# Performance work log

Measured on AMD Instinct MI355X. Metric: run time of the kernel, lower is better.

## Reference

```python
import jax, jax.numpy as jnp
import numpy as np
import math

B, S, D = 4, 2048, 1024      # batch, seq, d_model
E, F_EXP = 16, 512           # n_experts_ffn, d_expert_ffn
N_SHARED, K_FFN = 2, 4       # shared experts, routed top-k
N_ROUTED = E - N_SHARED


def setup_inputs() -> dict:
    key = jax.random.key(0)
    k0, k1, k2, k3, k4 = jax.random.split(key, 5)
    token_stream = jax.random.normal(k0, (B, S, D), jnp.float32)
    selection_input = jax.random.normal(k1, (B, S, D), jnp.float32)
    # init per reset_parameters (std_scale = 1.0)
    keys_w = jax.random.normal(k2, (E, D, F_EXP), jnp.float32) / math.sqrt(D)
    values_w = jax.random.normal(k3, (E, F_EXP, D), jnp.float32) / math.sqrt(E * F_EXP)
    expert_sel = jax.random.normal(k4, (E, D), jnp.float32) / math.sqrt(D)
    bias_ffn = jnp.zeros((E,), jnp.float32)  # load-balancing bias buffer
    return {
        "token_stream": token_stream,
        "selection_input": selection_input,
        "keys_w": keys_w,
        "values_w": values_w,
        "expert_sel": expert_sel,
        "bias_ffn": bias_ffn,
    }


def reference(token_stream, selection_input, keys_w, values_w, expert_sel, bias_ffn):
    # ---- routing: sigmoid affinity over all experts ----
    affinity = jax.nn.sigmoid(jnp.einsum("bsd,ed->bse", selection_input, expert_sel))  # [B,S,E]
    # top-k over routed experts (bias only affects ranking, not gathered affinity)
    _, routed_idx = jax.lax.top_k(affinity[..., :N_ROUTED] + bias_ffn[:N_ROUTED], K_FFN)  # [B,S,k]
    shared_idx = jnp.broadcast_to(
        jnp.arange(N_ROUTED, E, dtype=routed_idx.dtype), routed_idx.shape[:-1] + (N_SHARED,)
    )
    sel = jnp.concatenate([routed_idx, shared_idx], axis=-1)  # [B,S,K], K = k + shared
    aff_sel = jnp.take_along_axis(affinity, sel, axis=-1)     # [B,S,K]

    # ---- expert FFN (cvmm = gather / grouped GEMM / weighted scatter) ----
    # dense per-expert key projection, then gather selected experts
    scores_all = jnp.einsum("bsd,edf->bsef", token_stream, keys_w)        # [B,S,E,f]
    scores = jnp.take_along_axis(scores_all, sel[..., None], axis=2)      # [B,S,K,f]
    scores = jax.nn.silu(scores)

    # combine: out = sum_k aff_k * (scores_k @ values[sel_k])
    onehot = jax.nn.one_hot(sel, E, dtype=scores.dtype)                   # [B,S,K,E]
    dispatch = jnp.einsum("bskf,bske->bsef", scores * aff_sel[..., None], onehot)  # [B,S,E,f]
    out = jnp.einsum("bsef,efd->bsd", dispatch, values_w)                 # [B,S,D]
    return out, sel
```

## Files before the change

kernel.cpp:

```cpp
#include <hip/hip_runtime.h>

typedef short short8 __attribute__((ext_vector_type(8)));
typedef float f32x4 __attribute__((ext_vector_type(4)));
typedef unsigned short u16;

#define TOK_N 8192
#define DMODEL 1024
#define NEXP 16
#define FEXP 512
#define NROUTED 14
#define KSEL 6
#define MAXTILES 400

__device__ __forceinline__ u16 f2bf(float f) {
  unsigned u = __float_as_uint(f);
  u += 0x7fff + ((u >> 16) & 1);
  return (u16)(u >> 16);
}

typedef const __attribute__((address_space(1))) unsigned int* gas_p;
typedef __attribute__((address_space(3))) unsigned int* las_p;
__device__ __forceinline__ void gload_lds16(const void* g, void* l) {
  __builtin_amdgcn_global_load_lds((gas_p)g, (las_p)l, 16, 0, 0);
}

__global__ void cast_bf16_k(const float* __restrict__ in, u16* __restrict__ out, int n8) {
  int i = blockIdx.x * blockDim.x + threadIdx.x;
  if (i >= n8) return;
  const float4* p = (const float4*)(in + (size_t)i * 8);
  float4 a = p[0], b = p[1];
  short8 v;
  v[0] = (short)f2bf(a.x); v[1] = (short)f2bf(a.y); v[2] = (short)f2bf(a.z); v[3] = (short)f2bf(a.w);
  v[4] = (short)f2bf(b.x); v[5] = (short)f2bf(b.y); v[6] = (short)f2bf(b.z); v[7] = (short)f2bf(b.w);
  *(short8*)(out + (size_t)i * 8) = v;
}

__global__ void transpose_cast_k(const float* __restrict__ in, u16* __restrict__ out, int R, int C) {
  __shared__ u16 tile[32][33];
  int e = blockIdx.z;
  int c0 = blockIdx.x * 32, r0 = blockIdx.y * 32;
  int x = threadIdx.x, y = threadIdx.y;
  const float* ip = in + ((size_t)e * R + r0) * C + c0;
  #pragma unroll
  for (int i = 0; i < 4; i++)
    tile[y + 8 * i][x] = f2bf(ip[(size_t)(y + 8 * i) * C + x]);
  __syncthreads();
  u16* op = out + ((size_t)e * C + c0) * R + r0;
  #pragma unroll
  for (int i = 0; i < 4; i++)
    op[(size_t)(y + 8 * i) * R + x] = tile[x][y + 8 * i];
}

__global__ void routing_k(const float* __restrict__ selin, const float* __restrict__ esel,
                          const float* __restrict__ bias, float* __restrict__ out_sel,
                          unsigned* __restrict__ sel_pack, float* __restrict__ aff6) {
  int tok = blockIdx.x;
  int t = threadIdx.x;
  int e = t & 15, chunk = t >> 4;
  const float4* r4 = (const float4*)(selin + (size_t)tok * DMODEL + chunk * 64);
  const float4* w4 = (const float4*)(esel + (size_t)e * DMODEL + chunk * 64);
  float p = 0.f;
  #pragma unroll
  for (int i = 0; i < 16; i++) {
    float4 a = r4[i], b = w4[i];
    p += a.x * b.x + a.y * b.y + a.z * b.z + a.w * b.w;
  }
  __shared__ float part[16][17];
  __shared__ float aff[16];
  __shared__ float lbias[NROUTED];
  if (t < NROUTED) lbias[t] = bias[t];
  part[chunk][e] = p;
  __syncthreads();
  if (t < 16) {
    float s = 0.f;
    #pragma unroll
    for (int c = 0; c < 16; c++) s += part[c][t];
    aff[t] = 1.f / (1.f + expf(-s));
  }
  __syncthreads();
  if (t == 0) {
    unsigned pack = 0;
    unsigned taken = 0;
    #pragma unroll
    for (int k = 0; k < 4; k++) {
      float best = -3.4e38f; int bi = 0;
      for (int q = 0; q < NROUTED; q++) {
        if (taken & (1u << q)) continue;
        float v = aff[q] + lbias[q];
        if (v > best) { best = v; bi = q; }
      }
      taken |= 1u << bi;
      pack |= (unsigned)bi << (4 * k);
      out_sel[(size_t)tok * KSEL + k] = (float)bi;
      aff6[(size_t)tok * KSEL + k] = aff[bi];
    }
    pack |= 14u << 16; pack |= 15u << 20;
    out_sel[(size_t)tok * KSEL + 4] = 14.f;
    out_sel[(size_t)tok * KSEL + 5] = 15.f;
    aff6[(size_t)tok * KSEL + 4] = aff[14];
    aff6[(size_t)tok * KSEL + 5] = aff[15];
    sel_pack[tok] = pack;
  }
}

__global__ void scatter_k(const unsigned* __restrict__ sel_pack, const float* __restrict__ aff6,
                          int* __restrict__ counts, int* __restrict__ tokk,
                          float* __restrict__ affl) {
  __shared__ int lcnt[16], lbase[16], lcur[16];
  int t = threadIdx.x;
  int tok = blockIdx.x * 256 + t;
  if (t < 16) lcnt[t] = 0;
  __syncthreads();
  unsigned pack = sel_pack[tok];
  int eid[KSEL];
  #pragma unroll
  for (int k = 0; k < KSEL; k++) {
    eid[k] = (pack >> (4 * k)) & 15;
    atomicAdd(&lcnt[eid[k]], 1);
  }
  __syncthreads();
  if (t < 16) {
    lbase[t] = atomicAdd(&counts[t * 16], lcnt[t]);
    lcur[t] = 0;
  }
  __syncthreads();
  #pragma unroll
  for (int k = 0; k < KSEL; k++) {
    int e = eid[k];
    int slot = lbase[e] + atomicAdd(&lcur[e], 1);
    tokk[e * TOK_N + slot] = tok * 8 + k;
    affl[e * TOK_N + slot] = aff6[(size_t)tok * KSEL + k];
  }
}

__global__ void tilelist_k(const int* __restrict__ counts, int* __restrict__ tiles,
                           int* __restrict__ ntiles, int* __restrict__ pbase) {
  __shared__ int tc[16], pb[16];
  int t = threadIdx.x;
  if (t < 16) tc[t] = (counts[t * 16] + 127) >> 7;
  __syncthreads();
  if (t == 0) {
    int s = 0;
    for (int e = 0; e < 16; e++) { pb[e] = s; s += tc[e]; }
    *ntiles = s;
    int s2 = 0;
    for (int e = 0; e < 16; e++) { pbase[e] = s2; s2 += counts[e * 16]; }
  }
  __syncthreads();
  if (t < 16) {
    int b = pb[t], n = tc[t];
    for (int i = 0; i < n; i++) tiles[b + i] = t | (i << 8);
  }
}

template<int AK, int PASS>
__global__ __launch_bounds__(256, 2) void moe_gemm_k(
    const u16* __restrict__ Abase, const u16* __restrict__ Bbase,
    const int* __restrict__ counts, const int* __restrict__ tokk,
    const float* __restrict__ affl, const int* __restrict__ tiles,
    const int* __restrict__ ntiles, const int* __restrict__ pbase,
    u16* __restrict__ scores_out, float* __restrict__ out) {
  int slot = blockIdx.y;
  if (slot >= *ntiles) return;
  int desc = tiles[slot];
  int e = desc & 15;
  int m0 = (desc >> 8) << 7;
  int cnt = counts[e * 16];
  int pbe = pbase[e];
  int n0 = blockIdx.x * 128;
  int t = threadIdx.x;
  int lane = t & 63, w = t >> 6;
  int wr = w >> 1, wc = w & 1;

  __shared__ u16 Al[2][128][64];
  __shared__ u16 Bl[2][128][64];

  const int* tl = tokk + e * TOK_N + m0;
  const float* al = affl + e * TOK_N + m0;
  const u16* Bp = Bbase + (size_t)e * 524288;

  f32x4 acc[4][4];
  #pragma unroll
  for (int m = 0; m < 4; m++)
    #pragma unroll
    for (int n = 0; n < 4; n++)
      acc[m][n] = (f32x4){0.f, 0.f, 0.f, 0.f};

  int jj = lane & 7, rl = lane >> 3;
  const u16* ag[4]; const u16* bg[4];
  #pragma unroll
  for (int r = 0; r < 4; r++) {
    int row = r * 32 + w * 8 + rl;
    int lr = (m0 + row < cnt) ? row : 0;
    int ar;
    if (PASS == 2) {
      int tk = tl[lr];
      ar = tk >> 3;
    } else {
      ar = pbe + m0 + lr;
    }
    int cs = (jj ^ (row & 7)) * 8;
    ag[r] = Abase + (size_t)ar * AK + cs;
    bg[r] = Bp + (size_t)(n0 + row) * AK + cs;
  }

#define STAGE(B, K0)                                             \
  _Pragma("unroll")                                              \
  for (int r = 0; r < 4; r++) {                                  \
    gload_lds16(ag[r] + (K0), &Al[B][r * 32 + w * 8][0]);        \
    gload_lds16(bg[r] + (K0), &Bl[B][r * 32 + w * 8][0]);        \
  }

#define COMPUTE(B)                                                         \
  _Pragma("unroll")                                                        \
  for (int kk = 0; kk < 2; kk++) {                                         \
    int lc = kk * 4 + (lane >> 4);                                         \
    short8 af[4], bf[4];                                                   \
    _Pragma("unroll")                                                      \
    for (int m = 0; m < 4; m++) {                                          \
      int row = wr * 64 + m * 16 + (lane & 15);                            \
      af[m] = *(const short8*)&Al[B][row][(lc ^ (row & 7)) * 8];           \
    }                                                                      \
    _Pragma("unroll")                                                      \
    for (int n = 0; n < 4; n++) {                                          \
      int row = wc * 64 + n * 16 + (lane & 15);                            \
      bf[n] = *(const short8*)&Bl[B][row][(lc ^ (row & 7)) * 8];           \
    }                                                                      \
    _Pragma("unroll")                                                      \
    for (int m = 0; m < 4; m++)                                            \
      _Pragma("unroll")                                                    \
      for (int n = 0; n < 4; n++)                                          \
        acc[m][n] = __builtin_amdgcn_mfma_f32_16x16x32_bf16(af[m], bf[n],  \
                                                            acc[m][n], 0, 0, 0); \
  }

#define VWAIT8 asm volatile("s_waitcnt vmcnt(8)" ::: "memory")
#define VWAIT0 asm volatile("s_waitcnt vmcnt(0)" ::: "memory")
#define BARR  __builtin_amdgcn_s_barrier()
#define PIN   __builtin_amdgcn_sched_barrier(0)

  constexpr int NIT = AK / 64;
  STAGE(0, 0)
  #pragma unroll 1
  for (int it = 0; it < NIT - 2; it += 2) {
    STAGE(1, (it + 1) * 64)
    VWAIT8; BARR; PIN;
    COMPUTE(0)
    BARR; PIN;
    STAGE(0, (it + 2) * 64)
    VWAIT8; BARR; PIN;
    COMPUTE(1)
    BARR; PIN;
  }
  STAGE(1, (NIT - 1) * 64)
  VWAIT8; BARR; PIN;
  COMPUTE(0)
  BARR; PIN;
  VWAIT0; BARR; PIN;
  COMPUTE(1)

#undef STAGE
#undef COMPUTE
#undef VWAIT8
#undef VWAIT0
#undef BARR
#undef PIN

  int cbase = n0 + wc * 64 + (lane & 15);
  #pragma unroll
  for (int m = 0; m < 4; m++) {
    int rbase = wr * 64 + m * 16 + ((lane >> 4) << 2);
    #pragma unroll
    for (int q = 0; q < 4; q++) {
      int row = rbase + q;
      if (m0 + row >= cnt) continue;
      if (PASS == 2) {
        float aff = al[row];
        size_t base = (size_t)(pbe + m0 + row) * FEXP;
        #pragma unroll
        for (int n = 0; n < 4; n++) {
          float v = acc[m][n][q];
          float s = aff * v / (1.f + expf(-v));
          scores_out[base + cbase + n * 16] = f2bf(s);
        }
      } else {
        int tk = tl[row];
        size_t base = (size_t)(tk >> 3) * DMODEL;
        #pragma unroll
        for (int n = 0; n < 4; n++)
          atomicAdd(&out[base + cbase + n * 16], acc[m][n][q]);
      }
    }
  }
}

extern "C" void kernel_launch(void* const* d_in, const int* in_sizes, int n_in,
                              void* d_out, int out_size, void* d_ws, size_t ws_size,
                              hipStream_t stream) {
  (void)in_sizes; (void)n_in; (void)out_size; (void)ws_size;
  const float* token_stream    = (const float*)d_in[0];
  const float* selection_input = (const float*)d_in[1];
  const float* keys_w          = (const float*)d_in[2];
  const float* values_w        = (const float*)d_in[3];
  const float* expert_sel      = (const float*)d_in[4];
  const float* bias_ffn        = (const float*)d_in[5];

  float* out     = (float*)d_out;
  float* out_sel = out + (size_t)TOK_N * DMODEL;

  char* ws = (char*)d_ws;
  u16*      Xbf      = (u16*)(ws + 0);
  u16*      keysT    = (u16*)(ws + 16777216);
  u16*      valuesT  = (u16*)(ws + 33554432);
  u16*      scoresbf = (u16*)(ws + 50331648);
  int*      counts   = (int*)(ws + 100663296);
  int*      tokk     = (int*)(ws + 100664320);
  float*    affl     = (float*)(ws + 101188608);
  unsigned* sel_pack = (unsigned*)(ws + 101712896);
  float*    aff6     = (float*)(ws + 101745664);
  int*      tiles    = (int*)(ws + 101942272);
  int*      ntiles   = (int*)(ws + 101946368);
  int*      pbase    = (int*)(ws + 101946432);

  hipMemsetAsync(out, 0, (size_t)TOK_N * DMODEL * sizeof(float), stream);
  hipMemsetAsync(counts, 0, 1024, stream);

  cast_bf16_k<<<4096, 256, 0, stream>>>(token_stream, Xbf, TOK_N * DMODEL / 8);
  transpose_cast_k<<<dim3(16, 32, 16), dim3(32, 8), 0, stream>>>(keys_w, keysT, 1024, 512);
  transpose_cast_k<<<dim3(32, 16, 16), dim3(32, 8), 0, stream>>>(values_w, valuesT, 512, 1024);

  routing_k<<<TOK_N, 256, 0, stream>>>(selection_input, expert_sel, bias_ffn,
                                       out_sel, sel_pack, aff6);
  scatter_k<<<TOK_N / 256, 256, 0, stream>>>(sel_pack, aff6, counts, tokk, affl);
  tilelist_k<<<1, 64, 0, stream>>>(counts, tiles, ntiles, pbase);

  moe_gemm_k<1024, 2><<<dim3(4, MAXTILES), 256, 0, stream>>>(Xbf, keysT, counts, tokk, affl,
                                                             tiles, ntiles, pbase,
                                                             scoresbf, nullptr);
  moe_gemm_k<512, 3><<<dim3(8, MAXTILES), 256, 0, stream>>>(scoresbf, valuesT, counts, tokk, affl,
                                                            tiles, ntiles, pbase,
                                                            nullptr, out);
}
```

Measured before the change: 429.3 us.

## Switch MoE GEMM to triple-buffered K=32 stages with higher occupancy target

Replaces the double-buffered 64-wide K stage with a three-deep ring of 32-wide K stages, keeping two loads in flight while computing. LDS per block shrinks, so launch bounds now request 3 blocks per SM to raise occupancy. The XOR swizzle on LDS rows is dropped, which may bring back bank conflicts on the fragment reads. Each stage does half as many MFMAs per barrier, so synchronisation overhead per unit of work goes up.

```diff
diff --git a/kernel.cpp b/kernel.cpp
--- a/kernel.cpp
+++ b/kernel.cpp
@@ -154,7 +154,7 @@
 }
 
 template<int AK, int PASS>
-__global__ __launch_bounds__(256, 2) void moe_gemm_k(
+__global__ __launch_bounds__(256, 3) void moe_gemm_k(
     const u16* __restrict__ Abase, const u16* __restrict__ Bbase,
     const int* __restrict__ counts, const int* __restrict__ tokk,
     const float* __restrict__ affl, const int* __restrict__ tiles,
@@ -172,8 +172,8 @@
   int lane = t & 63, w = t >> 6;
   int wr = w >> 1, wc = w & 1;
 
-  __shared__ u16 Al[2][128][64];
-  __shared__ u16 Bl[2][128][64];
+  __shared__ u16 Al[3][128][32];
+  __shared__ u16 Bl[3][128][32];
 
   const int* tl = tokk + e * TOK_N + m0;
   const float* al = affl + e * TOK_N + m0;
@@ -186,11 +186,11 @@
     for (int n = 0; n < 4; n++)
       acc[m][n] = (f32x4){0.f, 0.f, 0.f, 0.f};
 
-  int jj = lane & 7, rl = lane >> 3;
-  const u16* ag[4]; const u16* bg[4];
-  #pragma unroll
-  for (int r = 0; r < 4; r++) {
-    int row = r * 32 + w * 8 + rl;
+  int rl4 = lane >> 2, c4 = (lane & 3) * 8;
+  const u16* ag[2]; const u16* bg[2];
+  #pragma unroll
+  for (int r = 0; r < 2; r++) {
+    int row = w * 32 + r * 16 + rl4;
     int lr = (m0 + row < cnt) ? row : 0;
     int ar;
     if (PASS == 2) {
@@ -199,33 +199,28 @@
     } else {
       ar = pbe + m0 + lr;
     }
-    int cs = (jj ^ (row & 7)) * 8;
-    ag[r] = Abase + (size_t)ar * AK + cs;
-    bg[r] = Bp + (size_t)(n0 + row) * AK + cs;
+    ag[r] = Abase + (size_t)ar * AK + c4;
+    bg[r] = Bp + (size_t)(n0 + row) * AK + c4;
   }
 
 #define STAGE(B, K0)                                             \
   _Pragma("unroll")                                              \
-  for (int r = 0; r < 4; r++) {                                  \
-    gload_lds16(ag[r] + (K0), &Al[B][r * 32 + w * 8][0]);        \
-    gload_lds16(bg[r] + (K0), &Bl[B][r * 32 + w * 8][0]);        \
+  for (int r = 0; r < 2; r++) {                                  \
+    gload_lds16(ag[r] + (K0), &Al[B][w * 32 + r * 16][0]);       \
+    gload_lds16(bg[r] + (K0), &Bl[B][w * 32 + r * 16][0]);       \
   }
 
 #define COMPUTE(B)                                                         \
-  _Pragma("unroll")                                                        \
-  for (int kk = 0; kk < 2; kk++) {                                         \
-    int lc = kk * 4 + (lane >> 4);                                         \
+  {                                                                        \
     short8 af[4], bf[4];                                                   \
     _Pragma("unroll")                                                      \
-    for (int m = 0; m < 4; m++) {                                          \
-      int row = wr * 64 + m * 16 + (lane & 15);                            \
-      af[m] = *(const short8*)&Al[B][row][(lc ^ (row & 7)) * 8];           \
-    }                                                                      \
+    for (int m = 0; m < 4; m++)                                            \
+      af[m] = *(const short8*)&Al[B][wr * 64 + m * 16 + (lane & 15)]       \
+                                  [(lane >> 4) * 8];                       \
     _Pragma("unroll")                                                      \
-    for (int n = 0; n < 4; n++) {                                          \
-      int row = wc * 64 + n * 16 + (lane & 15);                            \
-      bf[n] = *(const short8*)&Bl[B][row][(lc ^ (row & 7)) * 8];           \
-    }                                                                      \
+    for (int n = 0; n < 4; n++)                                            \
+      bf[n] = *(const short8*)&Bl[B][wc * 64 + n * 16 + (lane & 15)]       \
+                                  [(lane >> 4) * 8];                       \
     _Pragma("unroll")                                                      \
     for (int m = 0; m < 4; m++)                                            \
       _Pragma("unroll")                                                    \
@@ -235,33 +230,39 @@
   }
 
 #define VWAIT8 asm volatile("s_waitcnt vmcnt(8)" ::: "memory")
+#define VWAIT4 asm volatile("s_waitcnt vmcnt(4)" ::: "memory")
 #define VWAIT0 asm volatile("s_waitcnt vmcnt(0)" ::: "memory")
 #define BARR  __builtin_amdgcn_s_barrier()
 #define PIN   __builtin_amdgcn_sched_barrier(0)
 
-  constexpr int NIT = AK / 64;
+  constexpr int NP = AK / 32;
   STAGE(0, 0)
+  STAGE(1, 32)
+  STAGE(2, 64)
+  int bsel = 0;
   #pragma unroll 1
-  for (int it = 0; it < NIT - 2; it += 2) {
-    STAGE(1, (it + 1) * 64)
+  for (int p = 0; p < NP - 3; ++p) {
     VWAIT8; BARR; PIN;
-    COMPUTE(0)
+    COMPUTE(bsel)
     BARR; PIN;
-    STAGE(0, (it + 2) * 64)
-    VWAIT8; BARR; PIN;
-    COMPUTE(1)
-    BARR; PIN;
-  }
-  STAGE(1, (NIT - 1) * 64)
+    STAGE(bsel, (p + 3) * 32)
+    bsel = (bsel == 2) ? 0 : bsel + 1;
+  }
   VWAIT8; BARR; PIN;
-  COMPUTE(0)
+  COMPUTE(bsel)
   BARR; PIN;
+  bsel = (bsel == 2) ? 0 : bsel + 1;
+  VWAIT4; BARR; PIN;
+  COMPUTE(bsel)
+  BARR; PIN;
+  bsel = (bsel == 2) ? 0 : bsel + 1;
   VWAIT0; BARR; PIN;
-  COMPUTE(1)
+  COMPUTE(bsel)
 
 #undef STAGE
 #undef COMPUTE
 #undef VWAIT8
+#undef VWAIT4
 #undef VWAIT0
 #undef BARR
 #undef PIN
```

Result: slower. 438.9 us (+2.2%).

## Accumulate MoE output via packed bf16 atomics then cast to fp32

Applied to the files above, without the earlier changes.

The second grouped GEMM now scatters into a bf16 buffer that reuses the token-stream bf16 workspace, using packed bf16 atomic adds. Adjacent lanes exchange values with a shuffle so one lane issues a two-element atomic. A new kernel then widens the bf16 buffer into the fp32 output. This halves the atomic traffic and memset size compared with fp32 atomics, but accumulating up to six expert contributions in bf16 loses precision and adds a cast pass.

```diff
diff --git a/kernel.cpp b/kernel.cpp
--- a/kernel.cpp
+++ b/kernel.cpp
@@ -33,6 +33,22 @@
   v[0] = (short)f2bf(a.x); v[1] = (short)f2bf(a.y); v[2] = (short)f2bf(a.z); v[3] = (short)f2bf(a.w);
   v[4] = (short)f2bf(b.x); v[5] = (short)f2bf(b.y); v[6] = (short)f2bf(b.z); v[7] = (short)f2bf(b.w);
   *(short8*)(out + (size_t)i * 8) = v;
+}
+
+__global__ void cast_out_k(const u16* __restrict__ in, float* __restrict__ o) {
+  int i = blockIdx.x * 256 + threadIdx.x;
+  short8 v = *(const short8*)(in + (size_t)i * 8);
+  float4 a, b;
+  a.x = __uint_as_float(((unsigned)(u16)v[0]) << 16);
+  a.y = __uint_as_float(((unsigned)(u16)v[1]) << 16);
+  a.z = __uint_as_float(((unsigned)(u16)v[2]) << 16);
+  a.w = __uint_as_float(((unsigned)(u16)v[3]) << 16);
+  b.x = __uint_as_float(((unsigned)(u16)v[4]) << 16);
+  b.y = __uint_as_float(((unsigned)(u16)v[5]) << 16);
+  b.z = __uint_as_float(((unsigned)(u16)v[6]) << 16);
+  b.w = __uint_as_float(((unsigned)(u16)v[7]) << 16);
+  float4* op = (float4*)(o + (size_t)i * 8);
+  op[0] = a; op[1] = b;
 }
 
 __global__ void transpose_cast_k(const float* __restrict__ in, u16* __restrict__ out, int R, int C) {
@@ -159,7 +175,7 @@
     const int* __restrict__ counts, const int* __restrict__ tokk,
     const float* __restrict__ affl, const int* __restrict__ tiles,
     const int* __restrict__ ntiles, const int* __restrict__ pbase,
-    u16* __restrict__ scores_out, float* __restrict__ out) {
+    u16* __restrict__ scores_out) {
   int slot = blockIdx.y;
   if (slot >= *ntiles) return;
   int desc = tiles[slot];
@@ -287,8 +303,17 @@
         int tk = tl[row];
         size_t base = (size_t)(tk >> 3) * DMODEL;
         #pragma unroll
-        for (int n = 0; n < 4; n++)
-          atomicAdd(&out[base + cbase + n * 16], acc[m][n][q]);
+        for (int n = 0; n < 4; n++) {
+          float v = acc[m][n][q];
+          float v2 = __shfl_xor(v, 1);
+          if (!(lane & 1)) {
+            unsigned pk = (unsigned)f2bf(v) | ((unsigned)f2bf(v2) << 16);
+            u16* ap = scores_out + base + cbase + n * 16;
+            asm volatile("global_atomic_pk_add_bf16 %0, %1, off"
+                         :: "v"((unsigned long long)(uintptr_t)ap), "v"(pk)
+                         : "memory");
+          }
+        }
       }
     }
   }
@@ -321,8 +346,8 @@
   int*      tiles    = (int*)(ws + 101942272);
   int*      ntiles   = (int*)(ws + 101946368);
   int*      pbase    = (int*)(ws + 101946432);
-
-  hipMemsetAsync(out, 0, (size_t)TOK_N * DMODEL * sizeof(float), stream);
+  u16*      outbf    = Xbf;
+
   hipMemsetAsync(counts, 0, 1024, stream);
 
   cast_bf16_k<<<4096, 256, 0, stream>>>(token_stream, Xbf, TOK_N * DMODEL / 8);
@@ -335,9 +360,9 @@
   tilelist_k<<<1, 64, 0, stream>>>(counts, tiles, ntiles, pbase);
 
   moe_gemm_k<1024, 2><<<dim3(4, MAXTILES), 256, 0, stream>>>(Xbf, keysT, counts, tokk, affl,
-                                                             tiles, ntiles, pbase,
-                                                             scoresbf, nullptr);
+                                                             tiles, ntiles, pbase, scoresbf);
+  hipMemsetAsync(outbf, 0, (size_t)TOK_N * DMODEL * sizeof(u16), stream);
   moe_gemm_k<512, 3><<<dim3(8, MAXTILES), 256, 0, stream>>>(scoresbf, valuesT, counts, tokk, affl,
-                                                            tiles, ntiles, pbase,
-                                                            nullptr, out);
-}
+                                                            tiles, ntiles, pbase, outbf);
+  cast_out_k<<<4096, 256, 0, stream>>>(outbf, out);
+}
```

New measurement: 455.8 us. 6.2% more time.
